# Kernel optimization log

Measured on AMD Instinct MI355X. Metric: run time of the kernel, lower is better.

Reference implementation:

```python
import jax, jax.numpy as jnp
from jax import lax
import numpy as np

T, B, C, N, V = 128, 128, 128, 10, 5
TAU, VTH = 2.0, 0.8          # spikingjelly LIFNode defaults (tau=2, v_threshold=0.8 here)
BASE_THR, DECAY = 0.8, 0.8   # TrueDynamicThresholdLIF
EPS = 1e-5

@jax.custom_vjp
def atan_spike(x):
    # Heaviside forward, ATan surrogate backward (spikingjelly surrogate.ATan, alpha=2)
    return (x >= 0.0).astype(x.dtype)

def _as_fwd(x):
    return (x >= 0.0).astype(x.dtype), x

def _as_bwd(x, g):
    alpha = 2.0
    return (g * (alpha / 2.0) / (1.0 + (jnp.pi / 2.0 * alpha * x) ** 2),)

atan_spike.defvjp(_as_fwd, _as_bwd)

def group_norm(x, groups, gamma, beta):
    # x: [M, Cc, L]; biased variance, matches torch GroupNorm
    M, Cc, L = x.shape
    xr = x.reshape(M, groups, -1)
    mu = xr.mean(-1, keepdims=True)
    var = xr.var(-1, keepdims=True)
    xn = ((xr - mu) * lax.rsqrt(var + EPS)).reshape(M, Cc, L)
    return xn * gamma[None, :, None] + beta[None, :, None]

def lif_multistep(x_seq):
    # spikingjelly LIFNode, decay_input=True, hard reset to 0
    def step(v, x):
        v = v + (x - v) / TAU
        s = atan_spike(v - VTH)
        return v * (1.0 - s), s
    _, spikes = lax.scan(step, jnp.zeros_like(x_seq[0]), x_seq)
    return spikes

def ema_gate(x_seq, logit_alpha):
    a = jax.nn.sigmoid(logit_alpha)[0]
    def step(e, x):
        e = e * a + x * (1.0 - a)
        return e, e
    _, gate = lax.scan(step, jnp.zeros_like(x_seq[0]), x_seq)
    return gate

def dynamic_lif(x_seq, gate_seq):
    # v = v*decay + x; thr = base_thr*(2 - gate); hard reset to 0
    def step(v, xs):
        x, g = xs
        v = v * DECAY + x
        s = atan_spike(v - BASE_THR * (2.0 - g))
        return v * (1.0 - s), s
    _, spikes = lax.scan(step, jnp.zeros_like(x_seq[0]), (x_seq, gate_seq))
    return spikes

def setup_inputs() -> dict:
    key = jax.random.key(0)
    ks = jax.random.split(key, 5)
    return {
        "x": jax.random.uniform(ks[0], (T, B, C, N), jnp.float32),
        "conv1_w": jax.random.normal(ks[1], (C, C), jnp.float32) / np.float32(np.sqrt(C)),
        "norm1_g": jnp.ones((C,), jnp.float32),
        "norm1_b": jnp.zeros((C,), jnp.float32),
        "logit_alpha": jnp.full((1,), 2.1972246, jnp.float32),  # logit(0.9)
        "fusion_w": jax.random.normal(ks[2], (C, 2 * C), jnp.float32) / np.float32(np.sqrt(2 * C)),
        "fusion_gn_g": jnp.ones((C,), jnp.float32),
        "fusion_gn_b": jnp.zeros((C,), jnp.float32),
        "node_mixer_w": jax.random.normal(ks[3], (V, V), jnp.float32) / np.float32(np.sqrt(V)),
        "learnable_adj": jnp.eye(V, dtype=jnp.float32) + 0.01 * jax.random.normal(ks[4], (V, V), jnp.float32),
        "mixer_gn_g": jnp.ones((V,), jnp.float32),
        "mixer_gn_b": jnp.zeros((V,), jnp.float32),
    }

def reference(x, conv1_w, norm1_g, norm1_b, logit_alpha, fusion_w, fusion_gn_g,
              fusion_gn_b, node_mixer_w, learnable_adj, mixer_gn_g, mixer_gn_b):
    T_, B_, C_, N_ = x.shape
    V_ = N_ // 2
    # --- EMA causal neuromodulation gate ---
    gate = ema_gate(x, logit_alpha)                                  # [T,B,C,N]
    # --- conv1 (1x1 over channels) + GroupNorm(8, C) ---
    y = jnp.einsum('oc,tbcn->tbon', conv1_w, x)
    y = group_norm(y.reshape(T_ * B_, C_, N_), 8, norm1_g, norm1_b).reshape(T_, B_, C_, N_)
    # --- token mixer: dual-modality fusion ---
    acc, gyr = y[..., :V_], y[..., V_:]
    fused = jnp.concatenate([acc, gyr], axis=2)                      # [T,B,2C,V]
    z = jnp.einsum('oc,tbcv->tbov', fusion_w, fused)                 # [T,B,C,V]
    z = group_norm(z.reshape(T_ * B_, C_, V_), 1, fusion_gn_g, fusion_gn_b).reshape(T_, B_, C_, V_)
    z = lif_multistep(z)                                             # fusion LIF spikes
    # --- adjacency-masked node mixing (k=1 conv == VxV matmul) ---
    sym_adj = 0.5 * (learnable_adj + learnable_adj.T)
    w = node_mixer_w * jax.nn.sigmoid(sym_adj)                       # [V,V]
    m = jnp.einsum('uv,tbcv->tbcu', w, z)                            # [T,B,C,V]
    # GroupNorm(1, V) computed over [B*C, V, T] layout as in torch code
    m_bt = m.transpose(1, 2, 3, 0).reshape(B_ * C_, V_, T_)
    m_bt = group_norm(m_bt, 1, mixer_gn_g, mixer_gn_b)
    m = m_bt.reshape(B_, C_, V_, T_).transpose(3, 0, 1, 2)
    m = lif_multistep(m)                                             # topo LIF spikes
    mixed = jnp.concatenate([m, m], axis=-1)                         # dual-mode duplicate -> [T,B,C,N]
    # --- dynamic-threshold LIF driven by neuromod gate ---
    s = dynamic_lif(mixed, gate)
    # --- clamped residual ---
    return jnp.clip(x + s, 0.0, 1.0)
```

## Files before the change

kernel.cpp:

```cpp
#include <hip/hip_runtime.h>

#define T_ 128
#define B_ 128
#define C_ 128
#define N_ 10
#define V_ 5
#define XROW 1280
#define ZROW 640
#define ZSTRIDE 81920
#define XSTRIDE 163840
#define TQ 32
#define PAIRS_Q 4096

__global__ __launch_bounds__(256) void k_prep(const float* __restrict__ W1,
                                              const float* __restrict__ Wf,
                                              double* __restrict__ W1d,
                                              double* __restrict__ WfTd) {
  int i = blockIdx.x * 256 + threadIdx.x;
  if (i < 16384) {
    int c = i >> 7, o = i & 127;
    W1d[i] = (double)W1[o * 128 + c];
  } else if (i < 49152) {
    int k = i - 16384;
    int c2 = k >> 7, o = k & 127;
    WfTd[k] = (double)Wf[o * 256 + c2];
  }
}

__global__ __launch_bounds__(256) void k_gemm1(
    const float* __restrict__ x, const double* __restrict__ W1d,
    const float* __restrict__ g1, const float* __restrict__ b1,
    double* __restrict__ y_buf, int chunk_base)
{
  const int tid = threadIdx.x;
  const int o   = tid & 127;
  const int g2  = tid >> 7;
  const int plA = blockIdx.x * 4 + g2 * 2;
  const int plB = plA + 1;
  const int pgA = chunk_base + plA;
  const int pgB = chunk_base + plB;

  const int xbA = __builtin_amdgcn_readfirstlane(pgA * XROW);
  const int xbB = __builtin_amdgcn_readfirstlane(pgB * XROW);

  double accA[10], accB[10];
#pragma unroll
  for (int j = 0; j < 10; ++j) { accA[j] = 0.0; accB[j] = 0.0; }

#pragma unroll 2
  for (int c = 0; c < 128; ++c) {
    const double w = W1d[(c << 7) + o];
#pragma unroll
    for (int j = 0; j < 10; ++j) {
      accA[j] = fma(w, (double)x[xbA + c * 10 + j], accA[j]);
      accB[j] = fma(w, (double)x[xbB + c * 10 + j], accB[j]);
    }
  }

  const double gam = (double)g1[o], bet = (double)b1[o];
#pragma unroll
  for (int P = 0; P < 2; ++P) {
    double* acc = P ? accB : accA;
    double s = 0.0;
#pragma unroll
    for (int j = 0; j < 10; ++j) s += acc[j];
#pragma unroll
    for (int off = 1; off < 16; off <<= 1) s += __shfl_xor(s, off, 64);
    const double mu = s * (1.0 / 160.0);
    double sq = 0.0;
#pragma unroll
    for (int j = 0; j < 10; ++j) { double d = acc[j] - mu; sq = fma(d, d, sq); }
#pragma unroll
    for (int off = 1; off < 16; off <<= 1) sq += __shfl_xor(sq, off, 64);
    const double rstd = 1.0 / sqrt(sq * (1.0 / 160.0) + 1e-5);
    double* yo = y_buf + (size_t)(P ? plB : plA) * XROW + o * 10;
#pragma unroll
    for (int j = 0; j < 10; ++j) yo[j] = (acc[j] - mu) * rstd * gam + bet;
  }
}

__global__ __launch_bounds__(256) void k_gemm2(
    const double* __restrict__ y_buf, const double* __restrict__ WfTd,
    const float* __restrict__ fg, const float* __restrict__ fb,
    double* __restrict__ z_out, int chunk_base)
{
  __shared__ double red[2][2][2][2];
  const int tid  = threadIdx.x;
  const int o    = tid & 127;
  const int g2   = tid >> 7;
  const int wv   = (tid >> 6) & 1;
  const int lane = tid & 63;
  const int plA  = blockIdx.x * 4 + g2 * 2;
  const int plB  = plA + 1;

  const int ybA = __builtin_amdgcn_readfirstlane(plA * XROW);
  const int ybB = __builtin_amdgcn_readfirstlane(plB * XROW);

  double accA[5], accB[5];
#pragma unroll
  for (int v = 0; v < 5; ++v) { accA[v] = 0.0; accB[v] = 0.0; }

#pragma unroll 2
  for (int c = 0; c < 128; ++c) {
    const double wa = WfTd[(c << 7) + o];
    const double wb = WfTd[((c + 128) << 7) + o];
#pragma unroll
    for (int v = 0; v < 5; ++v) {
      accA[v] = fma(wa, y_buf[ybA + c * 10 + v], accA[v]);
      accA[v] = fma(wb, y_buf[ybA + c * 10 + 5 + v], accA[v]);
      accB[v] = fma(wa, y_buf[ybB + c * 10 + v], accB[v]);
      accB[v] = fma(wb, y_buf[ybB + c * 10 + 5 + v], accB[v]);
    }
  }

  double s0 = accA[0] + accA[1] + accA[2] + accA[3] + accA[4];
  double s1 = accB[0] + accB[1] + accB[2] + accB[3] + accB[4];
#pragma unroll
  for (int off = 1; off < 64; off <<= 1) {
    s0 += __shfl_xor(s0, off, 64);
    s1 += __shfl_xor(s1, off, 64);
  }
  if (lane == 0) { red[g2][0][0][wv] = s0; red[g2][1][0][wv] = s1; }
  __syncthreads();
  const double mu0 = (red[g2][0][0][0] + red[g2][0][0][1]) * (1.0 / 640.0);
  const double mu1 = (red[g2][1][0][0] + red[g2][1][0][1]) * (1.0 / 640.0);
  double q0 = 0.0, q1 = 0.0;
#pragma unroll
  for (int v = 0; v < 5; ++v) {
    double d0 = accA[v] - mu0; q0 = fma(d0, d0, q0);
    double d1 = accB[v] - mu1; q1 = fma(d1, d1, q1);
  }
#pragma unroll
  for (int off = 1; off < 64; off <<= 1) {
    q0 += __shfl_xor(q0, off, 64);
    q1 += __shfl_xor(q1, off, 64);
  }
  if (lane == 0) { red[g2][0][1][wv] = q0; red[g2][1][1][wv] = q1; }
  __syncthreads();
  const double rstd0 =
      1.0 / sqrt((red[g2][0][1][0] + red[g2][0][1][1]) * (1.0 / 640.0) + 1e-5);
  const double rstd1 =
      1.0 / sqrt((red[g2][1][1][0] + red[g2][1][1][1]) * (1.0 / 640.0) + 1e-5);

  const double gam = (double)fg[o], bet = (double)fb[o];
  double* zoA = z_out + (size_t)(chunk_base + plA) * ZROW + o * 5;
  double* zoB = z_out + (size_t)(chunk_base + plB) * ZROW + o * 5;
#pragma unroll
  for (int v = 0; v < 5; ++v) {
    zoA[v] = (accA[v] - mu0) * rstd0 * gam + bet;
    zoB[v] = (accB[v] - mu1) * rstd1 * gam + bet;
  }
}

__global__ __launch_bounds__(256) void k_temporal(
    const float* __restrict__ x, double* __restrict__ zm,
    const float* __restrict__ la, const float* __restrict__ nm,
    const float* __restrict__ adj, const float* __restrict__ mg,
    const float* __restrict__ mb, float* __restrict__ out)
{
  const int gid = blockIdx.x * 256 + threadIdx.x;
  const int bc = gid >> 3;
  const int u  = gid & 7;
  const bool act = (u < 5);

  double w[5];
#pragma unroll
  for (int v = 0; v < 5; ++v) {
    if (act) {
      double sa = 0.5 * ((double)adj[u * 5 + v] + (double)adj[v * 5 + u]);
      w[v] = (double)nm[u * 5 + v] * (1.0 / (1.0 + exp(-sa)));
    } else {
      w[v] = 0.0;
    }
  }
  const double aa  = 1.0 / (1.0 + exp(-(double)la[0]));
  const double oma = 1.0 - aa;
  const int lane  = threadIdx.x & 63;
  const int gbase = lane & ~7;
  const size_t zoff = (size_t)bc * 5 + u;

  double v1 = 0.0, ssum = 0.0, ssq = 0.0;
  double znext = act ? zm[zoff] : 0.0;
  for (int t = 0; t < T_; ++t) {
    const double zc = znext;
    if (t < T_ - 1)
      znext = act ? zm[zoff + (size_t)(t + 1) * ZSTRIDE] : 0.0;
    v1 = v1 + (zc - v1) * 0.5;
    double sp = (v1 - 0.8 >= 0.0) ? 1.0 : 0.0;
    v1 *= (1.0 - sp);
    double m = 0.0;
#pragma unroll
    for (int v = 0; v < 5; ++v) m = fma(w[v], __shfl(sp, gbase + v, 64), m);
    ssum += m;
    ssq = fma(m, m, ssq);
    if (act) zm[zoff + (size_t)t * ZSTRIDE] = m;
  }
#pragma unroll
  for (int off = 1; off < 8; off <<= 1) {
    ssum += __shfl_xor(ssum, off, 64);
    ssq  += __shfl_xor(ssq,  off, 64);
  }
  const double mu = ssum * (1.0 / 640.0);
  double var = ssq * (1.0 / 640.0) - mu * mu;
  const double rstd = 1.0 / sqrt(var + 1e-5);
  const double gam = act ? (double)mg[u] : 0.0;
  const double bet = act ? (double)mb[u] : 0.0;

  double v2 = 0.0, e0 = 0.0, e1 = 0.0, dd0 = 0.0, dd1 = 0.0;
  const size_t xoff = (size_t)bc * 10;
  double mnext = act ? zm[zoff] : 0.0;
  float x0n = act ? x[xoff + u] : 0.f;
  float x1n = act ? x[xoff + u + 5] : 0.f;
  for (int t = 0; t < T_; ++t) {
    const double mval = mnext;
    const float x0f = x0n, x1f = x1n;
    if (t < T_ - 1) {
      mnext = act ? zm[zoff + (size_t)(t + 1) * ZSTRIDE] : 0.0;
      x0n = act ? x[(size_t)(t + 1) * XSTRIDE + xoff + u] : 0.f;
      x1n = act ? x[(size_t)(t + 1) * XSTRIDE + xoff + u + 5] : 0.f;
    }
    double mn = (mval - mu) * rstd * gam + bet;
    v2 = v2 + (mn - v2) * 0.5;
    double s2 = (v2 - 0.8 >= 0.0) ? 1.0 : 0.0;
    v2 *= (1.0 - s2);

    e0 = e0 * aa + (double)x0f * oma;
    e1 = e1 * aa + (double)x1f * oma;

    dd0 = dd0 * 0.8 + s2;
    double sd0 = (dd0 - 0.8 * (2.0 - e0) >= 0.0) ? 1.0 : 0.0;
    dd0 *= (1.0 - sd0);

    dd1 = dd1 * 0.8 + s2;
    double sd1 = (dd1 - 0.8 * (2.0 - e1) >= 0.0) ? 1.0 : 0.0;
    dd1 *= (1.0 - sd1);

    if (act) {
      out[(size_t)t * XSTRIDE + xoff + u] =
          fminf(fmaxf(x0f + (float)sd0, 0.f), 1.f);
      out[(size_t)t * XSTRIDE + xoff + u + 5] =
          fminf(fmaxf(x1f + (float)sd1, 0.f), 1.f);
    }
  }
}

extern "C" void kernel_launch(void* const* d_in, const int* in_sizes, int n_in,
                              void* d_out, int out_size, void* d_ws, size_t ws_size,
                              hipStream_t stream) {
  const float* x   = (const float*)d_in[0];
  const float* W1  = (const float*)d_in[1];
  const float* g1  = (const float*)d_in[2];
  const float* b1  = (const float*)d_in[3];
  const float* la  = (const float*)d_in[4];
  const float* Wf  = (const float*)d_in[5];
  const float* fg  = (const float*)d_in[6];
  const float* fb  = (const float*)d_in[7];
  const float* nm  = (const float*)d_in[8];
  const float* adj = (const float*)d_in[9];
  const float* mg  = (const float*)d_in[10];
  const float* mb  = (const float*)d_in[11];
  float* outp = (float*)d_out;

  double* z_ws  = (double*)d_ws;
  double* y_buf = (double*)((char*)d_ws + 83886080);
  double* W1d   = (double*)((char*)d_ws + 83886080 + 41943040);
  double* WfTd  = (double*)((char*)d_ws + 83886080 + 41943040 + 131072);

  hipLaunchKernelGGL(k_prep, dim3(192), dim3(256), 0, stream, W1, Wf, W1d, WfTd);
  for (int q = 0; q < 4; ++q) {
    const int cb = q * PAIRS_Q;
    hipLaunchKernelGGL(k_gemm1, dim3(PAIRS_Q / 4), dim3(256), 0, stream,
                       x, W1d, g1, b1, y_buf, cb);
    hipLaunchKernelGGL(k_gemm2, dim3(PAIRS_Q / 4), dim3(256), 0, stream,
                       y_buf, WfTd, fg, fb, z_ws, cb);
  }
  hipLaunchKernelGGL(k_temporal, dim3(512), dim3(256), 0, stream,
                     x, z_ws, la, nm, adj, mg, mb, outp);
}
```

Baseline: 831.7 us.

## Stage weights in LDS, widen blocks to four pairs per group, pre-convert x

The two FP64 GEMM kernels now copy their transposed weights into shared memory as float and convert them to double on use. Each thread group now handles four (t,b) rows instead of two, so every weight load feeds more FMAs. A new pass converts each chunk of x to double ahead of GEMM1, and the chunk count adapts to the workspace size. The costs are a 64KB or 128KB LDS footprint, which limits occupancy, an extra kernel launch and round trip through memory per chunk, and more accumulator registers per thread.

After: 1.249 ms. +50.2%, slower.

```diff
diff --git a/kernel.cpp b/kernel.cpp
--- a/kernel.cpp
+++ b/kernel.cpp
@@ -9,146 +9,161 @@
 #define ZROW 640
 #define ZSTRIDE 81920
 #define XSTRIDE 163840
-#define TQ 32
-#define PAIRS_Q 4096
 
 __global__ __launch_bounds__(256) void k_prep(const float* __restrict__ W1,
                                               const float* __restrict__ Wf,
-                                              double* __restrict__ W1d,
-                                              double* __restrict__ WfTd) {
+                                              float* __restrict__ W1T,
+                                              float* __restrict__ WfT) {
   int i = blockIdx.x * 256 + threadIdx.x;
   if (i < 16384) {
     int c = i >> 7, o = i & 127;
-    W1d[i] = (double)W1[o * 128 + c];
+    W1T[i] = W1[o * 128 + c];
   } else if (i < 49152) {
     int k = i - 16384;
     int c2 = k >> 7, o = k & 127;
-    WfTd[k] = (double)Wf[o * 256 + c2];
-  }
-}
-
-__global__ __launch_bounds__(256) void k_gemm1(
-    const float* __restrict__ x, const double* __restrict__ W1d,
+    WfT[k] = Wf[o * 256 + c2];
+  }
+}
+
+__global__ __launch_bounds__(256) void k_xconv(const float* __restrict__ x,
+                                               double* __restrict__ xd,
+                                               long long base_elem) {
+  long long i = (long long)blockIdx.x * 256 + threadIdx.x;
+  float2 v = *(const float2*)(x + base_elem + 2 * i);
+  double2 d; d.x = (double)v.x; d.y = (double)v.y;
+  *(double2*)(xd + 2 * i) = d;
+}
+
+__global__ __launch_bounds__(512) void k_gemm1(
+    const double* __restrict__ x_d, const float* __restrict__ W1T,
     const float* __restrict__ g1, const float* __restrict__ b1,
-    double* __restrict__ y_buf, int chunk_base)
+    double* __restrict__ y_buf)
 {
+  __shared__ float w1t[16384];
   const int tid = threadIdx.x;
   const int o   = tid & 127;
-  const int g2  = tid >> 7;
-  const int plA = blockIdx.x * 4 + g2 * 2;
-  const int plB = plA + 1;
-  const int pgA = chunk_base + plA;
-  const int pgB = chunk_base + plB;
-
-  const int xbA = __builtin_amdgcn_readfirstlane(pgA * XROW);
-  const int xbB = __builtin_amdgcn_readfirstlane(pgB * XROW);
-
-  double accA[10], accB[10];
-#pragma unroll
-  for (int j = 0; j < 10; ++j) { accA[j] = 0.0; accB[j] = 0.0; }
+  const int grp = tid >> 7;
+  const int pl0 = blockIdx.x * 16 + grp * 4;
+
+  for (int i = tid; i < 16384; i += 512) w1t[i] = W1T[i];
+  __syncthreads();
+
+  int xb[4];
+#pragma unroll
+  for (int k = 0; k < 4; ++k)
+    xb[k] = __builtin_amdgcn_readfirstlane((pl0 + k) * XROW);
+
+  double acc[4][10];
+#pragma unroll
+  for (int k = 0; k < 4; ++k)
+#pragma unroll
+    for (int j = 0; j < 10; ++j) acc[k][j] = 0.0;
 
 #pragma unroll 2
   for (int c = 0; c < 128; ++c) {
-    const double w = W1d[(c << 7) + o];
-#pragma unroll
-    for (int j = 0; j < 10; ++j) {
-      accA[j] = fma(w, (double)x[xbA + c * 10 + j], accA[j]);
-      accB[j] = fma(w, (double)x[xbB + c * 10 + j], accB[j]);
+    const double w = (double)w1t[(c << 7) + o];
+#pragma unroll
+    for (int k = 0; k < 4; ++k) {
+      const double* xp = x_d + xb[k] + c * 10;
+#pragma unroll
+      for (int j = 0; j < 10; ++j)
+        acc[k][j] = fma(w, xp[j], acc[k][j]);
     }
   }
 
   const double gam = (double)g1[o], bet = (double)b1[o];
 #pragma unroll
-  for (int P = 0; P < 2; ++P) {
-    double* acc = P ? accB : accA;
+  for (int k = 0; k < 4; ++k) {
     double s = 0.0;
 #pragma unroll
-    for (int j = 0; j < 10; ++j) s += acc[j];
+    for (int j = 0; j < 10; ++j) s += acc[k][j];
 #pragma unroll
     for (int off = 1; off < 16; off <<= 1) s += __shfl_xor(s, off, 64);
     const double mu = s * (1.0 / 160.0);
     double sq = 0.0;
 #pragma unroll
-    for (int j = 0; j < 10; ++j) { double d = acc[j] - mu; sq = fma(d, d, sq); }
+    for (int j = 0; j < 10; ++j) { double d = acc[k][j] - mu; sq = fma(d, d, sq); }
 #pragma unroll
     for (int off = 1; off < 16; off <<= 1) sq += __shfl_xor(sq, off, 64);
     const double rstd = 1.0 / sqrt(sq * (1.0 / 160.0) + 1e-5);
-    double* yo = y_buf + (size_t)(P ? plB : plA) * XROW + o * 10;
-#pragma unroll
-    for (int j = 0; j < 10; ++j) yo[j] = (acc[j] - mu) * rstd * gam + bet;
-  }
-}
-
-__global__ __launch_bounds__(256) void k_gemm2(
-    const double* __restrict__ y_buf, const double* __restrict__ WfTd,
+    double* yo = y_buf + (size_t)(pl0 + k) * XROW + o * 10;
+#pragma unroll
+    for (int j = 0; j < 10; ++j) yo[j] = (acc[k][j] - mu) * rstd * gam + bet;
+  }
+}
+
+__global__ __launch_bounds__(512) void k_gemm2(
+    const double* __restrict__ y_buf, const float* __restrict__ WfT,
     const float* __restrict__ fg, const float* __restrict__ fb,
     double* __restrict__ z_out, int chunk_base)
 {
-  __shared__ double red[2][2][2][2];
+  __shared__ float wft[32768];
+  __shared__ double red[4][4][2][2];
   const int tid  = threadIdx.x;
   const int o    = tid & 127;
-  const int g2   = tid >> 7;
+  const int grp  = tid >> 7;
   const int wv   = (tid >> 6) & 1;
   const int lane = tid & 63;
-  const int plA  = blockIdx.x * 4 + g2 * 2;
-  const int plB  = plA + 1;
-
-  const int ybA = __builtin_amdgcn_readfirstlane(plA * XROW);
-  const int ybB = __builtin_amdgcn_readfirstlane(plB * XROW);
-
-  double accA[5], accB[5];
-#pragma unroll
-  for (int v = 0; v < 5; ++v) { accA[v] = 0.0; accB[v] = 0.0; }
+  const int pl0  = blockIdx.x * 16 + grp * 4;
+
+  for (int i = tid; i < 32768; i += 512) wft[i] = WfT[i];
+  __syncthreads();
+
+  int yb[4];
+#pragma unroll
+  for (int k = 0; k < 4; ++k)
+    yb[k] = __builtin_amdgcn_readfirstlane((pl0 + k) * XROW);
+
+  double acc[4][5];
+#pragma unroll
+  for (int k = 0; k < 4; ++k)
+#pragma unroll
+    for (int v = 0; v < 5; ++v) acc[k][v] = 0.0;
 
 #pragma unroll 2
-  for (int c = 0; c < 128; ++c) {
-    const double wa = WfTd[(c << 7) + o];
-    const double wb = WfTd[((c + 128) << 7) + o];
-#pragma unroll
-    for (int v = 0; v < 5; ++v) {
-      accA[v] = fma(wa, y_buf[ybA + c * 10 + v], accA[v]);
-      accA[v] = fma(wb, y_buf[ybA + c * 10 + 5 + v], accA[v]);
-      accB[v] = fma(wa, y_buf[ybB + c * 10 + v], accB[v]);
-      accB[v] = fma(wb, y_buf[ybB + c * 10 + 5 + v], accB[v]);
-    }
-  }
-
-  double s0 = accA[0] + accA[1] + accA[2] + accA[3] + accA[4];
-  double s1 = accB[0] + accB[1] + accB[2] + accB[3] + accB[4];
-#pragma unroll
-  for (int off = 1; off < 64; off <<= 1) {
-    s0 += __shfl_xor(s0, off, 64);
-    s1 += __shfl_xor(s1, off, 64);
-  }
-  if (lane == 0) { red[g2][0][0][wv] = s0; red[g2][1][0][wv] = s1; }
+  for (int c2 = 0; c2 < 256; ++c2) {
+    const double w = (double)wft[(c2 << 7) + o];
+    const int yoff = (c2 & 127) * 10 + (c2 >> 7) * 5;
+#pragma unroll
+    for (int k = 0; k < 4; ++k) {
+      const double* yp = y_buf + yb[k] + yoff;
+#pragma unroll
+      for (int v = 0; v < 5; ++v)
+        acc[k][v] = fma(w, yp[v], acc[k][v]);
+    }
+  }
+
+  double mu[4];
+#pragma unroll
+  for (int k = 0; k < 4; ++k) {
+    double s = acc[k][0] + acc[k][1] + acc[k][2] + acc[k][3] + acc[k][4];
+#pragma unroll
+    for (int off = 1; off < 64; off <<= 1) s += __shfl_xor(s, off, 64);
+    if (lane == 0) red[grp][k][0][wv] = s;
+  }
   __syncthreads();
-  const double mu0 = (red[g2][0][0][0] + red[g2][0][0][1]) * (1.0 / 640.0);
-  const double mu1 = (red[g2][1][0][0] + red[g2][1][0][1]) * (1.0 / 640.0);
-  double q0 = 0.0, q1 = 0.0;
-#pragma unroll
-  for (int v = 0; v < 5; ++v) {
-    double d0 = accA[v] - mu0; q0 = fma(d0, d0, q0);
-    double d1 = accB[v] - mu1; q1 = fma(d1, d1, q1);
-  }
-#pragma unroll
-  for (int off = 1; off < 64; off <<= 1) {
-    q0 += __shfl_xor(q0, off, 64);
-    q1 += __shfl_xor(q1, off, 64);
-  }
-  if (lane == 0) { red[g2][0][1][wv] = q0; red[g2][1][1][wv] = q1; }
+#pragma unroll
+  for (int k = 0; k < 4; ++k)
+    mu[k] = (red[grp][k][0][0] + red[grp][k][0][1]) * (1.0 / 640.0);
+#pragma unroll
+  for (int k = 0; k < 4; ++k) {
+    double q = 0.0;
+#pragma unroll
+    for (int v = 0; v < 5; ++v) { double d = acc[k][v] - mu[k]; q = fma(d, d, q); }
+#pragma unroll
+    for (int off = 1; off < 64; off <<= 1) q += __shfl_xor(q, off, 64);
+    if (lane == 0) red[grp][k][1][wv] = q;
+  }
   __syncthreads();
-  const double rstd0 =
-      1.0 / sqrt((red[g2][0][1][0] + red[g2][0][1][1]) * (1.0 / 640.0) + 1e-5);
-  const double rstd1 =
-      1.0 / sqrt((red[g2][1][1][0] + red[g2][1][1][1]) * (1.0 / 640.0) + 1e-5);
-
   const double gam = (double)fg[o], bet = (double)fb[o];
-  double* zoA = z_out + (size_t)(chunk_base + plA) * ZROW + o * 5;
-  double* zoB = z_out + (size_t)(chunk_base + plB) * ZROW + o * 5;
-#pragma unroll
-  for (int v = 0; v < 5; ++v) {
-    zoA[v] = (accA[v] - mu0) * rstd0 * gam + bet;
-    zoB[v] = (accB[v] - mu1) * rstd1 * gam + bet;
+#pragma unroll
+  for (int k = 0; k < 4; ++k) {
+    const double rstd =
+        1.0 / sqrt((red[grp][k][1][0] + red[grp][k][1][1]) * (1.0 / 640.0) + 1e-5);
+    double* zo = z_out + (size_t)(chunk_base + pl0 + k) * ZROW + o * 5;
+#pragma unroll
+    for (int v = 0; v < 5; ++v)
+      zo[v] = (acc[k][v] - mu[k]) * rstd * gam + bet;
   }
 }
 
@@ -261,18 +276,27 @@
   const float* mb  = (const float*)d_in[11];
   float* outp = (float*)d_out;
 
+  const size_t zB = 83886080ull;
+  const size_t need32 = zB + 2ull * 41943040 + 196608;
+  const int nChunks = (ws_size >= need32) ? 4 : 8;
+  const int PQ = 16384 / nChunks;
+  const size_t pqB = (size_t)PQ * XROW * sizeof(double);
+
   double* z_ws  = (double*)d_ws;
-  double* y_buf = (double*)((char*)d_ws + 83886080);
-  double* W1d   = (double*)((char*)d_ws + 83886080 + 41943040);
-  double* WfTd  = (double*)((char*)d_ws + 83886080 + 41943040 + 131072);
-
-  hipLaunchKernelGGL(k_prep, dim3(192), dim3(256), 0, stream, W1, Wf, W1d, WfTd);
-  for (int q = 0; q < 4; ++q) {
-    const int cb = q * PAIRS_Q;
-    hipLaunchKernelGGL(k_gemm1, dim3(PAIRS_Q / 4), dim3(256), 0, stream,
-                       x, W1d, g1, b1, y_buf, cb);
-    hipLaunchKernelGGL(k_gemm2, dim3(PAIRS_Q / 4), dim3(256), 0, stream,
-                       y_buf, WfTd, fg, fb, z_ws, cb);
+  double* y_buf = (double*)((char*)d_ws + zB);
+  double* x_d   = (double*)((char*)d_ws + zB + pqB);
+  float*  W1T   = (float*)((char*)d_ws + zB + 2 * pqB);
+  float*  WfT   = (float*)((char*)d_ws + zB + 2 * pqB + 65536);
+
+  hipLaunchKernelGGL(k_prep, dim3(192), dim3(256), 0, stream, W1, Wf, W1T, WfT);
+  for (int q = 0; q < nChunks; ++q) {
+    const int cb = q * PQ;
+    hipLaunchKernelGGL(k_xconv, dim3(PQ * 640 / 256), dim3(256), 0, stream,
+                       x, x_d, (long long)cb * XROW);
+    hipLaunchKernelGGL(k_gemm1, dim3(PQ / 16), dim3(512), 0, stream,
+                       x_d, W1T, g1, b1, y_buf);
+    hipLaunchKernelGGL(k_gemm2, dim3(PQ / 16), dim3(512), 0, stream,
+                       y_buf, WfT, fg, fb, z_ws, cb);
   }
   hipLaunchKernelGGL(k_temporal, dim3(512), dim3(256), 0, stream,
                      x, z_ws, la, nm, adj, mg, mb, outp);
```
